# Performance work log

Measured on AMD Instinct MI355X. Metric: run time of the kernel, lower is better.

## Reference

```python
import jax, jax.numpy as jnp
import numpy as np

H = 32
W = 32
N = H * W            # num_patches = 1024
DIM = 512
HEADS = 8
DH = 64              # dim_head
INNER = HEADS * DH
B = 4
GATE = -2.0          # fixed, requires_grad=False in the torch module
NEG_THRESH = 0.9


def _rel_pos_index_dis():
    # mirrors relative_pos_index_dis(height=32, weight=32)
    coords = np.stack(np.meshgrid(np.arange(H), np.arange(W), indexing='ij'))  # [2,H,W]
    flat = coords.reshape(2, -1)                      # [2, N]
    rel = flat[:, :, None] - flat[:, None, :]         # [2, N, N]
    rel = rel.transpose(1, 2, 0).copy()               # [N, N, 2]
    dis = (rel[..., 0].astype(np.float32) / H) ** 2 + (rel[..., 1].astype(np.float32) / W) ** 2
    rel[..., 0] += H - 1
    rel[..., 1] += W - 1
    rel[..., 0] *= 2 * W - 1
    idx = rel.sum(-1)
    return idx.astype(np.int32), dis.astype(np.float32)


def setup_inputs() -> dict:
    key = jax.random.key(0)
    ks = jax.random.split(key, 6)
    rpi, dis = _rel_pos_index_dis()
    return {
        'x': jax.random.normal(ks[0], (B, N, DIM), dtype=jnp.float32),
        'prob': jax.random.uniform(ks[1], (B, N), dtype=jnp.float32),
        'w_qkv': jax.random.normal(ks[2], (DIM, 3 * INNER), dtype=jnp.float32) * 0.02,
        'rpb_table': jax.random.normal(ks[3], ((2 * H - 1) * (2 * W - 1), HEADS), dtype=jnp.float32) * 0.02,
        'headsita': jnp.arange(1, HEADS + 1, dtype=jnp.float32) * 0.1,
        'w_thresh': jax.random.normal(ks[4], (DH,), dtype=jnp.float32) * 0.02,
        'w_out': jax.random.normal(ks[5], (INNER, DIM), dtype=jnp.float32) * 0.02,
        'b_out': jnp.zeros((DIM,), dtype=jnp.float32),
        'rpi': jnp.asarray(rpi),
        'dis': jnp.asarray(dis),
    }


def reference(x, prob, w_qkv, rpb_table, headsita, w_thresh, w_out, b_out, rpi, dis):
    b, n, _ = x.shape
    h = headsita.shape[0]
    d = w_thresh.shape[0]
    scale = d ** -0.5

    qkv = x @ w_qkv                                            # [b, n, 3*h*d]
    q, k, v = jnp.split(qkv, 3, axis=-1)
    to_heads = lambda t: t.reshape(b, n, h, d).transpose(0, 2, 1, 3)  # [b, h, n, d]
    q, k, v = to_heads(q), to_heads(k), to_heads(v)

    dots0 = jnp.einsum('bhid,bhjd->bhij', q, k) * scale        # [b, h, n, n]

    # RPE: table lookup bias + learned Gaussian distance bias
    rpb = rpb_table[rpi.reshape(-1)].reshape(n, n, h).transpose(2, 0, 1)  # [h, n, n]
    factor = 1.0 / (2.0 * headsita ** 2 + 1e-6)                # [h]
    pos = jnp.exp(-factor[:, None, None] * dis[None, :, :])    # [h, n, n]
    dots = dots0 + rpb[None] + 0.01 * pos[None]

    attn = jax.nn.softmax(dots, axis=-1)                       # [b, h, n, n]
    attn_max = attn.max(axis=-1)                               # [b, h, n]
    attn_min = attn.min(axis=-1)

    # per-query learned threshold, gated by sigmoid(gate)
    t = jax.nn.sigmoid(jnp.einsum('bhnd,d->bhn', q, w_thresh)) * jax.nn.sigmoid(GATE)
    thresh = attn_min + t * (attn_max - attn_min)               # [b, h, n]

    record = (attn - thresh[..., None] > 0).astype(attn.dtype)  # hard 0/1 mask
    # rows (queries) whose prob >= neg_thresh are fully zeroed (as in the torch code)
    record = record * (prob < NEG_THRESH)[:, None, :, None].astype(attn.dtype)

    deno = jnp.sum(attn * record, axis=-1)                      # [b, h, n]
    attn_p = attn * record / (deno[..., None] + 1e-6)

    out = jnp.einsum('bhij,bhjd->bhid', attn_p, v)              # [b, h, n, d]
    out = out.transpose(0, 2, 1, 3).reshape(b, n, h * d)
    out = out @ w_out + b_out                                   # [b, n, dim]
    return out, jax.nn.softmax(dots0, axis=-1)
```

## Files before the change

### kernel.cpp

```cpp
#include <hip/hip_runtime.h>


__device__ __forceinline__ float wsum(float v) {
#pragma unroll
  for (int off = 32; off > 0; off >>= 1) v += __shfl_xor(v, off, 64);
  return v;
}
__device__ __forceinline__ float wmaxr(float v) {
#pragma unroll
  for (int off = 32; off > 0; off >>= 1) v = fmaxf(v, __shfl_xor(v, off, 64));
  return v;
}
__device__ __forceinline__ float wminr(float v) {
#pragma unroll
  for (int off = 32; off > 0; off >>= 1) v = fminf(v, __shfl_xor(v, off, 64));
  return v;
}

__global__ void build_btab(const float* __restrict__ rpb,
                           const float* __restrict__ headsita,
                           float* __restrict__ btab) {
  const int h = blockIdx.y;
  const int flat = blockIdx.x * 256 + threadIdx.x;
  if (flat >= 3969) return;
  const float sita = headsita[h];
  const float factor = 1.0f / (2.0f * sita * sita + 1e-6f);
  const int dy = flat / 63 - 31;
  const int dx = flat % 63 - 31;
  const float fy = (float)dy * 0.03125f, fx = (float)dx * 0.03125f;
  btab[h * 3969 + flat] =
      rpb[(size_t)flat * 8 + h] + 0.01f * __expf(-factor * (fy * fy + fx * fx));
}

__global__ __launch_bounds__(256, 4) void gemm_f32_128(
    const float* __restrict__ A, const float* __restrict__ Bm,
    float* __restrict__ C, int M, int N, int K) {
  __shared__ float As[16][132];
  __shared__ float Bs[16][132];
  const int t = threadIdx.x;
  const int bm = blockIdx.y * 128;
  const int bn = blockIdx.x * 128;
  const int tx = t & 15;
  const int ty = t >> 4;

  float acc[8][8];
#pragma unroll
  for (int i = 0; i < 8; ++i)
#pragma unroll
    for (int j = 0; j < 8; ++j) acc[i][j] = 0.0f;

  const int mr = t >> 1;
  const int kc = (t & 1) * 8;
  const int kr = t >> 4;
  const int nc = (t & 15) * 8;

  for (int k0 = 0; k0 < K; k0 += 16) {
    const float4* asrc = (const float4*)&A[(size_t)(bm + mr) * K + k0 + kc];
    const float4 a0 = asrc[0], a1 = asrc[1];
    const float4* bsrc = (const float4*)&Bm[(size_t)(k0 + kr) * N + bn + nc];
    const float4 b0 = bsrc[0], b1 = bsrc[1];
    __syncthreads();
    As[kc + 0][mr] = a0.x; As[kc + 1][mr] = a0.y;
    As[kc + 2][mr] = a0.z; As[kc + 3][mr] = a0.w;
    As[kc + 4][mr] = a1.x; As[kc + 5][mr] = a1.y;
    As[kc + 6][mr] = a1.z; As[kc + 7][mr] = a1.w;
    *(float4*)&Bs[kr][nc] = b0;
    *(float4*)&Bs[kr][nc + 4] = b1;
    __syncthreads();
#pragma unroll
    for (int kk = 0; kk < 16; ++kk) {
      const float4 aLo = *(const float4*)&As[kk][ty * 4];
      const float4 aHi = *(const float4*)&As[kk][64 + ty * 4];
      const float4 bLo = *(const float4*)&Bs[kk][tx * 4];
      const float4 bHi = *(const float4*)&Bs[kk][64 + tx * 4];
      const float av[8] = {aLo.x, aLo.y, aLo.z, aLo.w, aHi.x, aHi.y, aHi.z, aHi.w};
      const float bv[8] = {bLo.x, bLo.y, bLo.z, bLo.w, bHi.x, bHi.y, bHi.z, bHi.w};
#pragma unroll
      for (int i = 0; i < 8; ++i)
#pragma unroll
        for (int j = 0; j < 8; ++j) acc[i][j] += av[i] * bv[j];
    }
  }

#pragma unroll
  for (int i = 0; i < 8; ++i) {
    const int row = bm + ((i < 4) ? (ty * 4 + i) : (64 + ty * 4 + (i - 4)));
    float4 lo, hi;
    lo.x = acc[i][0]; lo.y = acc[i][1]; lo.z = acc[i][2]; lo.w = acc[i][3];
    hi.x = acc[i][4]; hi.y = acc[i][5]; hi.z = acc[i][6]; hi.w = acc[i][7];
    *(float4*)&C[(size_t)row * N + bn + tx * 4] = lo;
    *(float4*)&C[(size_t)row * N + bn + 64 + tx * 4] = hi;
  }
}

__global__ __launch_bounds__(256, 3) void attn_fused(
    const float* __restrict__ qkv,
    const float* __restrict__ prob,
    const float* __restrict__ btab,
    const float* __restrict__ w_thresh,
    float* __restrict__ out2,
    float* __restrict__ attnout)
{
  __shared__ float kv_lds[128 * 64];
  __shared__ float q_t[64 * 36];
  __shared__ float multi[2080];

  const int t = threadIdx.x;
  const int w = t >> 6, l = t & 63;
  const int itile = blockIdx.x;
  const int bh = blockIdx.y;
  const int b = bh >> 3, h = bh & 7;
  const int i0 = itile * 32;
  const int yi = itile;

  const float* bsl = btab + h * 3969 + yi * 63;
#pragma unroll
  for (int c = 0; c < 8; ++c) {
    const int e = c * 256 + t;
    if (e < 2016) multi[e] = bsl[e];
  }
#pragma unroll
  for (int c = 0; c < 8; ++c) {
    const int idx = c * 256 + t;
    const int row = idx >> 6, d = idx & 63;
    q_t[d * 36 + row] = qkv[(size_t)(b * 1024 + i0 + row) * 1536 + h * 64 + d];
  }
  __syncthreads();

  const float wt = w_thresh[l];
#pragma unroll
  for (int r = 0; r < 8; ++r) {
    const int row = w * 8 + r;
    const float v = wsum(q_t[l * 36 + row] * wt);
    float tv = (1.0f / (1.0f + __expf(-v))) * 0.11920292202211755f;
    tv += (prob[b * 1024 + i0 + row] >= 0.9f) ? 2.0f : 0.0f;
    multi[2048 + w * 8 + r] = tv;
  }

  float s[8][16];
#pragma unroll
  for (int r = 0; r < 8; ++r)
#pragma unroll
    for (int tt = 0; tt < 16; ++tt) s[r][tt] = 0.0f;

  const size_t kbase = (size_t)b * 1024 * 1536 + 512 + h * 64;
#pragma unroll
  for (int jt = 0; jt < 8; ++jt) {
    __syncthreads();
#pragma unroll
    for (int c = 0; c < 8; ++c) {
      const int f = (c * 256 + t) * 4;
      const int j = f >> 6, dd = f & 63;
      const float4 v4 = *(const float4*)&qkv[kbase + (size_t)(jt * 128 + j) * 1536 + dd];
      *(float4*)&kv_lds[j * 64 + 4 * ((dd >> 2) ^ (j & 15))] = v4;
    }
    __syncthreads();
#pragma unroll 4
    for (int d0 = 0; d0 < 64; d0 += 4) {
      const int g = 4 * ((d0 >> 2) ^ (l & 15));
      const float4 ka = *(const float4*)&kv_lds[l * 64 + g];
      const float4 kb = *(const float4*)&kv_lds[(64 + l) * 64 + g];
      const float ka4[4] = {ka.x, ka.y, ka.z, ka.w};
      const float kb4[4] = {kb.x, kb.y, kb.z, kb.w};
#pragma unroll
      for (int i = 0; i < 4; ++i) {
        const float4 qA = *(const float4*)&q_t[(d0 + i) * 36 + w * 8];
        const float4 qB = *(const float4*)&q_t[(d0 + i) * 36 + w * 8 + 4];
        const float qa[8] = {qA.x, qA.y, qA.z, qA.w, qB.x, qB.y, qB.z, qB.w};
#pragma unroll
        for (int r = 0; r < 8; ++r) {
          s[r][jt * 2 + 0] += qa[r] * ka4[i];
          s[r][jt * 2 + 1] += qa[r] * kb4[i];
        }
      }
    }
  }

  const size_t o2base = ((size_t)(b * 8 + h)) << 20;
#pragma unroll
  for (int r = 0; r < 8; ++r) {
#pragma unroll
    for (int tt = 0; tt < 16; ++tt) s[r][tt] *= 0.125f;
    float m = -1e30f;
#pragma unroll
    for (int tt = 0; tt < 16; ++tt) m = fmaxf(m, s[r][tt]);
    m = wmaxr(m);
    float sum = 0.0f;
#pragma unroll
    for (int tt = 0; tt < 16; ++tt) sum += __expf(s[r][tt] - m);
    sum = wsum(sum);
    const float inv = 1.0f / sum;
    float* orow = out2 + o2base + (size_t)(i0 + w * 8 + r) * 1024;
#pragma unroll
    for (int tt = 0; tt < 16; ++tt)
      __builtin_nontemporal_store(__expf(s[r][tt] - m) * inv, &orow[tt * 64 + l]);
  }

#pragma unroll
  for (int r = 0; r < 8; ++r) {
    const int xi = (w * 8 + r) & 31;
#pragma unroll
    for (int tt = 0; tt < 16; ++tt) {
      const int j = tt * 64 + l;
      const int yj = j >> 5, xj = j & 31;
      s[r][tt] += multi[(31 - yj) * 63 + (xi - xj + 31)];
    }
  }

#pragma unroll
  for (int r = 0; r < 8; ++r) {
    float m = -1e30f, mn = 1e30f;
#pragma unroll
    for (int tt = 0; tt < 16; ++tt) { m = fmaxf(m, s[r][tt]); mn = fminf(mn, s[r][tt]); }
    m = wmaxr(m); mn = wminr(mn);
    float sum = 0.0f;
#pragma unroll
    for (int tt = 0; tt < 16; ++tt) { const float e = __expf(s[r][tt] - m); s[r][tt] = e; sum += e; }
    sum = wsum(sum);
    const float emin = __expf(mn - m);
    const float tv = multi[2048 + w * 8 + r];
    const float th_e = emin + tv * (1.0f - emin);
    float deno = 0.0f;
#pragma unroll
    for (int tt = 0; tt < 16; ++tt) {
      const float a = (s[r][tt] > th_e) ? s[r][tt] : 0.0f;
      s[r][tt] = a;
      deno += a;
    }
    deno = wsum(deno);
    const float invden = 1.0f / (deno + 1e-6f * sum);
#pragma unroll
    for (int tt = 0; tt < 16; ++tt) s[r][tt] *= invden;
  }

  float outv[8];
#pragma unroll
  for (int r = 0; r < 8; ++r) outv[r] = 0.0f;
  const size_t vbase = (size_t)b * 1024 * 1536 + 1024 + h * 64;
#pragma unroll
  for (int jt = 0; jt < 8; ++jt) {
    __syncthreads();
#pragma unroll
    for (int c = 0; c < 8; ++c) {
      const int f = (c * 256 + t) * 4;
      const int j = f >> 6, dd = f & 63;
      const float4 v4 = *(const float4*)&qkv[vbase + (size_t)(jt * 128 + j) * 1536 + dd];
      const float vv4[4] = {v4.x, v4.y, v4.z, v4.w};
#pragma unroll
      for (int i = 0; i < 4; ++i)
        kv_lds[(dd + i) * 128 + 4 * ((j >> 2) ^ ((dd + i) & 15)) + (j & 3)] = vv4[i];
    }
    __syncthreads();
#pragma unroll
    for (int h2 = 0; h2 < 2; ++h2) {
#pragma unroll
      for (int r = 0; r < 8; ++r) multi[w * 512 + r * 64 + l] = s[r][jt * 2 + h2];
#pragma unroll 4
      for (int j0 = 0; j0 < 64; j0 += 4) {
        const int jc = h2 * 64 + j0;
        const float4 vv = *(const float4*)&kv_lds[l * 128 + 4 * ((jc >> 2) ^ (l & 15))];
        const float vvv[4] = {vv.x, vv.y, vv.z, vv.w};
#pragma unroll
        for (int r = 0; r < 8; ++r) {
          const float4 p4 = *(const float4*)&multi[w * 512 + r * 64 + j0];
          outv[r] += p4.x * vvv[0] + p4.y * vvv[1] + p4.z * vvv[2] + p4.w * vvv[3];
        }
      }
    }
  }
#pragma unroll
  for (int r = 0; r < 8; ++r)
    attnout[(size_t)(b * 1024 + i0 + w * 8 + r) * 512 + h * 64 + l] = outv[r];
}

__global__ __launch_bounds__(256, 4) void gemm_f32_64_bias(
    const float* __restrict__ A, const float* __restrict__ Bm,
    const float* __restrict__ bias, float* __restrict__ C,
    int M, int N, int K) {
  __shared__ float As[16][68];
  __shared__ float Bs[16][68];
  const int t = threadIdx.x;
  const int bm = blockIdx.y * 64;
  const int bn = blockIdx.x * 64;
  const int tx = t & 15;
  const int ty = t >> 4;

  float acc[4][4];
#pragma unroll
  for (int i = 0; i < 4; ++i)
#pragma unroll
    for (int j = 0; j < 4; ++j) acc[i][j] = 0.0f;

  const int amr = t >> 2;
  const int akc = (t & 3) * 4;
  const int bkr = t >> 4;
  const int bnc = (t & 15) * 4;

  for (int k0 = 0; k0 < K; k0 += 16) {
    const float4 a0 = *(const float4*)&A[(size_t)(bm + amr) * K + k0 + akc];
    const float4 b0 = *(const float4*)&Bm[(size_t)(k0 + bkr) * N + bn + bnc];
    __syncthreads();
    As[akc + 0][amr] = a0.x; As[akc + 1][amr] = a0.y;
    As[akc + 2][amr] = a0.z; As[akc + 3][amr] = a0.w;
    *(float4*)&Bs[bkr][bnc] = b0;
    __syncthreads();
#pragma unroll
    for (int kk = 0; kk < 16; ++kk) {
      const float4 av = *(const float4*)&As[kk][ty * 4];
      const float4 bv = *(const float4*)&Bs[kk][tx * 4];
      const float aa[4] = {av.x, av.y, av.z, av.w};
      const float bb[4] = {bv.x, bv.y, bv.z, bv.w};
#pragma unroll
      for (int i = 0; i < 4; ++i)
#pragma unroll
        for (int j = 0; j < 4; ++j) acc[i][j] += aa[i] * bb[j];
    }
  }

  const float4 bi = *(const float4*)&bias[bn + tx * 4];
#pragma unroll
  for (int i = 0; i < 4; ++i) {
    float4 o;
    o.x = acc[i][0] + bi.x; o.y = acc[i][1] + bi.y;
    o.z = acc[i][2] + bi.z; o.w = acc[i][3] + bi.w;
    *(float4*)&C[(size_t)(bm + ty * 4 + i) * N + bn + tx * 4] = o;
  }
}

extern "C" void kernel_launch(void* const* d_in, const int* in_sizes, int n_in,
                              void* d_out, int out_size, void* d_ws, size_t ws_size,
                              hipStream_t stream) {
  const float* x        = (const float*)d_in[0];
  const float* prob     = (const float*)d_in[1];
  const float* w_qkv    = (const float*)d_in[2];
  const float* rpb      = (const float*)d_in[3];
  const float* headsita = (const float*)d_in[4];
  const float* w_thresh = (const float*)d_in[5];
  const float* w_out    = (const float*)d_in[6];
  const float* b_out    = (const float*)d_in[7];

  float* out  = (float*)d_out;
  float* out2 = out + (size_t)4 * 1024 * 512;

  float* qkv     = (float*)d_ws;
  float* attnout = qkv + (size_t)4 * 1024 * 1536;
  float* btab    = attnout + (size_t)4 * 1024 * 512;

  build_btab<<<dim3(16, 8), 256, 0, stream>>>(rpb, headsita, btab);

  gemm_f32_128<<<dim3(1536 / 128, 4096 / 128), 256, 0, stream>>>(
      x, w_qkv, qkv, 4096, 1536, 512);

  attn_fused<<<dim3(32, 32), 256, 0, stream>>>(
      qkv, prob, btab, w_thresh, out2, attnout);

  gemm_f32_64_bias<<<dim3(512 / 64, 4096 / 64), 256, 0, stream>>>(
      attnout, w_out, b_out, out, 4096, 512, 512);
}
```

Baseline: 590.9 us.

## Remap attention block order, use scalar XOR swizzle for K/V LDS, cache exps

New measurement: 634.6 us. +7.4%, slower.

```diff
diff --git a/kernel.cpp b/kernel.cpp
--- a/kernel.cpp
+++ b/kernel.cpp
@@ -32,7 +32,7 @@
       rpb[(size_t)flat * 8 + h] + 0.01f * __expf(-factor * (fy * fy + fx * fx));
 }
 
-__global__ __launch_bounds__(256, 4) void gemm_f32_128(
+__global__ __launch_bounds__(256) void gemm_f32_128(
     const float* __restrict__ A, const float* __restrict__ Bm,
     float* __restrict__ C, int M, int N, int K) {
   __shared__ float As[16][132];
@@ -103,12 +103,14 @@
 {
   __shared__ float kv_lds[128 * 64];
   __shared__ float q_t[64 * 36];
-  __shared__ float multi[2080];
+  __shared__ float multi[2048];
 
   const int t = threadIdx.x;
   const int w = t >> 6, l = t & 63;
-  const int itile = blockIdx.x;
-  const int bh = blockIdx.y;
+  const int id = blockIdx.y * 32 + blockIdx.x;
+  const int work = (id & 7) * 128 + (id >> 3);
+  const int bh = work >> 5;
+  const int itile = work & 31;
   const int b = bh >> 3, h = bh & 7;
   const int i0 = itile * 32;
   const int yi = itile;
@@ -128,13 +130,14 @@
   __syncthreads();
 
   const float wt = w_thresh[l];
+  float tval[8];
 #pragma unroll
   for (int r = 0; r < 8; ++r) {
     const int row = w * 8 + r;
     const float v = wsum(q_t[l * 36 + row] * wt);
     float tv = (1.0f / (1.0f + __expf(-v))) * 0.11920292202211755f;
     tv += (prob[b * 1024 + i0 + row] >= 0.9f) ? 2.0f : 0.0f;
-    multi[2048 + w * 8 + r] = tv;
+    tval[r] = tv;
   }
 
   float s[8][16];
@@ -144,6 +147,7 @@
     for (int tt = 0; tt < 16; ++tt) s[r][tt] = 0.0f;
 
   const size_t kbase = (size_t)b * 1024 * 1536 + 512 + h * 64;
+  const int swl = l & 31;
 #pragma unroll
   for (int jt = 0; jt < 8; ++jt) {
     __syncthreads();
@@ -152,26 +156,24 @@
       const int f = (c * 256 + t) * 4;
       const int j = f >> 6, dd = f & 63;
       const float4 v4 = *(const float4*)&qkv[kbase + (size_t)(jt * 128 + j) * 1536 + dd];
-      *(float4*)&kv_lds[j * 64 + 4 * ((dd >> 2) ^ (j & 15))] = v4;
-    }
-    __syncthreads();
-#pragma unroll 4
-    for (int d0 = 0; d0 < 64; d0 += 4) {
-      const int g = 4 * ((d0 >> 2) ^ (l & 15));
-      const float4 ka = *(const float4*)&kv_lds[l * 64 + g];
-      const float4 kb = *(const float4*)&kv_lds[(64 + l) * 64 + g];
-      const float ka4[4] = {ka.x, ka.y, ka.z, ka.w};
-      const float kb4[4] = {kb.x, kb.y, kb.z, kb.w};
-#pragma unroll
-      for (int i = 0; i < 4; ++i) {
-        const float4 qA = *(const float4*)&q_t[(d0 + i) * 36 + w * 8];
-        const float4 qB = *(const float4*)&q_t[(d0 + i) * 36 + w * 8 + 4];
-        const float qa[8] = {qA.x, qA.y, qA.z, qA.w, qB.x, qB.y, qB.z, qB.w};
-#pragma unroll
-        for (int r = 0; r < 8; ++r) {
-          s[r][jt * 2 + 0] += qa[r] * ka4[i];
-          s[r][jt * 2 + 1] += qa[r] * kb4[i];
-        }
+      const int sw = j & 31;
+      kv_lds[j * 64 + ((dd + 0) ^ sw)] = v4.x;
+      kv_lds[j * 64 + ((dd + 1) ^ sw)] = v4.y;
+      kv_lds[j * 64 + ((dd + 2) ^ sw)] = v4.z;
+      kv_lds[j * 64 + ((dd + 3) ^ sw)] = v4.w;
+    }
+    __syncthreads();
+#pragma unroll 8
+    for (int d = 0; d < 64; ++d) {
+      const float kv0 = kv_lds[l * 64 + (d ^ swl)];
+      const float kv1 = kv_lds[(64 + l) * 64 + (d ^ swl)];
+      const float4 qA = *(const float4*)&q_t[d * 36 + w * 8];
+      const float4 qB = *(const float4*)&q_t[d * 36 + w * 8 + 4];
+      const float qa[8] = {qA.x, qA.y, qA.z, qA.w, qB.x, qB.y, qB.z, qB.w};
+#pragma unroll
+      for (int r = 0; r < 8; ++r) {
+        s[r][jt * 2 + 0] += qa[r] * kv0;
+        s[r][jt * 2 + 1] += qa[r] * kv1;
       }
     }
   }
@@ -185,15 +187,16 @@
 #pragma unroll
     for (int tt = 0; tt < 16; ++tt) m = fmaxf(m, s[r][tt]);
     m = wmaxr(m);
+    float e[16];
     float sum = 0.0f;
 #pragma unroll
-    for (int tt = 0; tt < 16; ++tt) sum += __expf(s[r][tt] - m);
+    for (int tt = 0; tt < 16; ++tt) { e[tt] = __expf(s[r][tt] - m); sum += e[tt]; }
     sum = wsum(sum);
     const float inv = 1.0f / sum;
     float* orow = out2 + o2base + (size_t)(i0 + w * 8 + r) * 1024;
 #pragma unroll
     for (int tt = 0; tt < 16; ++tt)
-      __builtin_nontemporal_store(__expf(s[r][tt] - m) * inv, &orow[tt * 64 + l]);
+      __builtin_nontemporal_store(e[tt] * inv, &orow[tt * 64 + l]);
   }
 
 #pragma unroll
@@ -218,8 +221,7 @@
     for (int tt = 0; tt < 16; ++tt) { const float e = __expf(s[r][tt] - m); s[r][tt] = e; sum += e; }
     sum = wsum(sum);
     const float emin = __expf(mn - m);
-    const float tv = multi[2048 + w * 8 + r];
-    const float th_e = emin + tv * (1.0f - emin);
+    const float th_e = emin + tval[r] * (1.0f - emin);
     float deno = 0.0f;
 #pragma unroll
     for (int tt = 0; tt < 16; ++tt) {
@@ -245,10 +247,11 @@
       const int f = (c * 256 + t) * 4;
       const int j = f >> 6, dd = f & 63;
       const float4 v4 = *(const float4*)&qkv[vbase + (size_t)(jt * 128 + j) * 1536 + dd];
-      const float vv4[4] = {v4.x, v4.y, v4.z, v4.w};
-#pragma unroll
-      for (int i = 0; i < 4; ++i)
-        kv_lds[(dd + i) * 128 + 4 * ((j >> 2) ^ ((dd + i) & 15)) + (j & 3)] = vv4[i];
+      const int sw = j & 31;
+      kv_lds[j * 64 + ((dd + 0) ^ sw)] = v4.x;
+      kv_lds[j * 64 + ((dd + 1) ^ sw)] = v4.y;
+      kv_lds[j * 64 + ((dd + 2) ^ sw)] = v4.z;
+      kv_lds[j * 64 + ((dd + 3) ^ sw)] = v4.w;
     }
     __syncthreads();
 #pragma unroll
@@ -257,13 +260,15 @@
       for (int r = 0; r < 8; ++r) multi[w * 512 + r * 64 + l] = s[r][jt * 2 + h2];
 #pragma unroll 4
       for (int j0 = 0; j0 < 64; j0 += 4) {
-        const int jc = h2 * 64 + j0;
-        const float4 vv = *(const float4*)&kv_lds[l * 128 + 4 * ((jc >> 2) ^ (l & 15))];
-        const float vvv[4] = {vv.x, vv.y, vv.z, vv.w};
+        const int jb = h2 * 64 + j0;
+        const float v0 = kv_lds[(jb + 0) * 64 + (l ^ ((jb + 0) & 31))];
+        const float v1 = kv_lds[(jb + 1) * 64 + (l ^ ((jb + 1) & 31))];
+        const float v2 = kv_lds[(jb + 2) * 64 + (l ^ ((jb + 2) & 31))];
+        const float v3 = kv_lds[(jb + 3) * 64 + (l ^ ((jb + 3) & 31))];
 #pragma unroll
         for (int r = 0; r < 8; ++r) {
           const float4 p4 = *(const float4*)&multi[w * 512 + r * 64 + j0];
-          outv[r] += p4.x * vvv[0] + p4.y * vvv[1] + p4.z * vvv[2] + p4.w * vvv[3];
+          outv[r] += p4.x * v0 + p4.y * v1 + p4.z * v2 + p4.w * v3;
         }
       }
     }
@@ -273,7 +278,7 @@
     attnout[(size_t)(b * 1024 + i0 + w * 8 + r) * 512 + h * 64 + l] = outv[r];
 }
 
-__global__ __launch_bounds__(256, 4) void gemm_f32_64_bias(
+__global__ __launch_bounds__(256) void gemm_f32_64_bias(
     const float* __restrict__ A, const float* __restrict__ Bm,
     const float* __restrict__ bias, float* __restrict__ C,
     int M, int N, int K) {
```
